# Kernel optimization log

Measured on AMD Instinct MI355X. Metric: run time of the kernel, lower is better.

The kernel has to match this reference:

```python
import jax, jax.numpy as jnp
import numpy as np

# init kwargs baked as constants: crop_height -> depth dim, crop_length -> H, crop_width -> W
CROP_D, CROP_H, CROP_W = 16, 16, 16
EXTRAP = 0.0


def setup_inputs() -> dict:
    key = jax.random.key(0)
    k1, k2, k3 = jax.random.split(key, 3)
    N, C, D, H, W = 8, 32, 64, 64, 64
    NB = 256
    image = jax.random.normal(k1, (N, C, D, H, W), dtype=jnp.float32)
    # boxes: normalized (x1, y1, z1, x2, y2, z2) with lo <= hi per axis
    raw = jax.random.uniform(k2, (NB, 3, 2), dtype=jnp.float32)
    lo = jnp.min(raw, axis=2)
    hi = jnp.max(raw, axis=2)
    boxes = jnp.concatenate([lo, hi], axis=1)  # [NB, 6]
    box_ind = jax.random.randint(k3, (NB,), 0, N, dtype=jnp.int32)
    return {"image": image, "boxes": boxes, "box_ind": box_ind}


def _coords(lo, hi, L, c):
    # lo, hi: [nb] normalized box edges; returns [nb, c] continuous source coords
    if c > 1:
        i = jnp.arange(c, dtype=lo.dtype)
        step = (hi - lo) * (L - 1) / (c - 1)          # [nb]
        return lo[:, None] * (L - 1) + i[None, :] * step[:, None]
    return (0.5 * (lo + hi) * (L - 1))[:, None]


def _lerp_idx(coord, L):
    valid = (coord >= 0) & (coord <= L - 1)
    c = jnp.clip(coord, 0, L - 1)
    i0 = jnp.floor(c).astype(jnp.int32)
    i1 = jnp.minimum(i0 + 1, L - 1)
    frac = c - i0.astype(coord.dtype)
    return i0, i1, frac, valid


def reference(image, boxes, box_ind):
    N, C, D, H, W = image.shape
    x1, y1, z1, x2, y2, z2 = [boxes[:, k] for k in range(6)]
    zc = _coords(z1, z2, D, CROP_D)  # [nb, cd]
    yc = _coords(y1, y2, H, CROP_H)  # [nb, ch]
    xc = _coords(x1, x2, W, CROP_W)  # [nb, cw]
    z0, z1i, fz, vz = _lerp_idx(zc, D)
    y0, y1i, fy, vy = _lerp_idx(yc, H)
    x0, x1i, fx, vx = _lerp_idx(xc, W)

    img = jnp.moveaxis(image, 1, -1)  # [N, D, H, W, C] -> channels-last gather
    b = box_ind[:, None, None, None]

    def g(zi, yi, xi):
        # [nb, cd, ch, cw, C]
        return img[b, zi[:, :, None, None], yi[:, None, :, None], xi[:, None, None, :], :]

    fz_ = fz[:, :, None, None, None]
    fy_ = fy[:, None, :, None, None]
    fx_ = fx[:, None, None, :, None]

    c00 = g(z0, y0, x0) * (1 - fx_) + g(z0, y0, x1i) * fx_
    c01 = g(z0, y1i, x0) * (1 - fx_) + g(z0, y1i, x1i) * fx_
    c10 = g(z1i, y0, x0) * (1 - fx_) + g(z1i, y0, x1i) * fx_
    c11 = g(z1i, y1i, x0) * (1 - fx_) + g(z1i, y1i, x1i) * fx_
    c0 = c00 * (1 - fy_) + c01 * fy_
    c1 = c10 * (1 - fy_) + c11 * fy_
    out = c0 * (1 - fz_) + c1 * fz_  # [nb, cd, ch, cw, C]

    valid = (vz[:, :, None, None] & vy[:, None, :, None] & vx[:, None, None, :])[..., None]
    out = jnp.where(valid, out, jnp.asarray(EXTRAP, out.dtype))
    return jnp.moveaxis(out, -1, 1)  # [nb, C, cd, ch, cw]
```

## Files before the change

kernel.cpp:

```cpp
#include <hip/hip_runtime.h>

#define NBOX 256
#define NC   32
#define ND   64
#define NH   64
#define NW   64
#define CD   16
#define CH   16
#define CW   16
#define NXCD 8

__global__ __launch_bounds__(256) void CropAndResize3D_89481348645400_kernel(
    const float* __restrict__ image,
    const float* __restrict__ boxes,
    const int*   __restrict__ box_ind,
    float*       __restrict__ out)
{
    const int nwg_per_xcd = (NBOX * CD) / NXCD;
    const int hw  = blockIdx.x;
    const int blk = (hw & (NXCD - 1)) * nwg_per_xcd + (hw >> 3);

    const int b = blk >> 4;
    const int z = blk & 15;
    const int t = threadIdx.x;
    const int y = t >> 4;
    const int x = t & 15;

    const float bx1 = boxes[b * 6 + 0];
    const float by1 = boxes[b * 6 + 1];
    const float bz1 = boxes[b * 6 + 2];
    const float bx2 = boxes[b * 6 + 3];
    const float by2 = boxes[b * 6 + 4];
    const float bz2 = boxes[b * 6 + 5];
    const int   n   = box_ind[b];

    const float zstep = (bz2 - bz1) * (float)(ND - 1) / (float)(CD - 1);
    const float ystep = (by2 - by1) * (float)(NH - 1) / (float)(CH - 1);
    const float xstep = (bx2 - bx1) * (float)(NW - 1) / (float)(CW - 1);
    const float zc = bz1 * (float)(ND - 1) + (float)z * zstep;
    const float yc = by1 * (float)(NH - 1) + (float)y * ystep;
    const float xc = bx1 * (float)(NW - 1) + (float)x * xstep;

    const bool valid =
        (zc >= 0.0f) && (zc <= (float)(ND - 1)) &&
        (yc >= 0.0f) && (yc <= (float)(NH - 1)) &&
        (xc >= 0.0f) && (xc <= (float)(NW - 1));

    const float zq = fminf(fmaxf(zc, 0.0f), (float)(ND - 1));
    const float yq = fminf(fmaxf(yc, 0.0f), (float)(NH - 1));
    const float xq = fminf(fmaxf(xc, 0.0f), (float)(NW - 1));
    const int z0 = (int)floorf(zq);
    const int y0 = (int)floorf(yq);
    const int x0 = (int)floorf(xq);
    const int z1 = min(z0 + 1, ND - 1);
    const int y1 = min(y0 + 1, NH - 1);
    const int x1 = min(x0 + 1, NW - 1);
    const float fz = zq - (float)z0;
    const float fy = yq - (float)y0;
    const float fx = xq - (float)x0;
    const float gz = 1.0f - fz, gy = 1.0f - fy, gx = 1.0f - fx;

    const float w000 = gz * gy * gx, w001 = gz * gy * fx;
    const float w010 = gz * fy * gx, w011 = gz * fy * fx;
    const float w100 = fz * gy * gx, w101 = fz * gy * fx;
    const float w110 = fz * fy * gx, w111 = fz * fy * fx;

    const int o00 = (z0 * NH + y0) * NW;
    const int o01 = (z0 * NH + y1) * NW;
    const int o10 = (z1 * NH + y0) * NW;
    const int o11 = (z1 * NH + y1) * NW;

    const float* img = image + (size_t)n * (NC * ND * NH * NW);
    float* op = out + (size_t)b * (NC * CD * CH * CW) + (z * CH + y) * CW + x;

    #pragma unroll 8
    for (int c = 0; c < NC; ++c) {
        const float* p = img + (size_t)c * (ND * NH * NW);
        float v = p[o00 + x0] * w000 + p[o00 + x1] * w001
                + p[o01 + x0] * w010 + p[o01 + x1] * w011
                + p[o10 + x0] * w100 + p[o10 + x1] * w101
                + p[o11 + x0] * w110 + p[o11 + x1] * w111;
        v = valid ? v : 0.0f;
        __builtin_nontemporal_store(v, op + c * (CD * CH * CW));
    }
}

extern "C" void kernel_launch(void* const* d_in, const int* in_sizes, int n_in,
                              void* d_out, int out_size, void* d_ws, size_t ws_size,
                              hipStream_t stream) {
    const float* image   = (const float*)d_in[0];
    const float* boxes   = (const float*)d_in[1];
    const int*   box_ind = (const int*)d_in[2];
    float*       out     = (float*)d_out;

    const int blocks = NBOX * CD;
    CropAndResize3D_89481348645400_kernel<<<blocks, 256, 0, stream>>>(
        image, boxes, box_ind, out);
}
```

Before: 138.1 us.

## Stage full source rows in LDS with double-buffered float4 loads per channel

Each block now cooperatively loads, per channel, the 64 needed source rows (the 16 y0/y1 row pairs at z0 and z1) as full 64-wide rows into padded shared memory using float4 loads. Threads then do their eight-tap trilinear interpolation from LDS. Loading whole rows avoids many scattered 4-byte global gathers. The next channel's loads are issued into registers while the current channel computes, which overlaps latency. The cost is fetching whole 64-wide rows even when the box spans few x columns, plus four barriers per channel pair.

```diff
diff --git a/kernel.cpp b/kernel.cpp
--- a/kernel.cpp
+++ b/kernel.cpp
@@ -9,6 +9,9 @@
 #define CH   16
 #define CW   16
 #define NXCD 8
+#define HW_  (NH * NW)
+#define DHW  (ND * NH * NW)
+#define PAD  68
 
 __global__ __launch_bounds__(256) void CropAndResize3D_89481348645400_kernel(
     const float* __restrict__ image,
@@ -16,15 +19,17 @@
     const int*   __restrict__ box_ind,
     float*       __restrict__ out)
 {
+    __shared__ float sh[64 * PAD];
+
     const int nwg_per_xcd = (NBOX * CD) / NXCD;
     const int hw  = blockIdx.x;
     const int blk = (hw & (NXCD - 1)) * nwg_per_xcd + (hw >> 3);
 
     const int b = blk >> 4;
     const int z = blk & 15;
-    const int t = threadIdx.x;
-    const int y = t >> 4;
-    const int x = t & 15;
+    const int t  = threadIdx.x;
+    const int ty = t >> 4;
+    const int tx = t & 15;
 
     const float bx1 = boxes[b * 6 + 0];
     const float by1 = boxes[b * 6 + 1];
@@ -34,55 +39,109 @@
     const float bz2 = boxes[b * 6 + 5];
     const int   n   = box_ind[b];
 
-    const float zstep = (bz2 - bz1) * (float)(ND - 1) / (float)(CD - 1);
-    const float ystep = (by2 - by1) * (float)(NH - 1) / (float)(CH - 1);
-    const float xstep = (bx2 - bx1) * (float)(NW - 1) / (float)(CW - 1);
-    const float zc = bz1 * (float)(ND - 1) + (float)z * zstep;
-    const float yc = by1 * (float)(NH - 1) + (float)y * ystep;
-    const float xc = bx1 * (float)(NW - 1) + (float)x * xstep;
+    const float zstep = (bz2 - bz1) * 63.0f / 15.0f;
+    const float ystep = (by2 - by1) * 63.0f / 15.0f;
+    const float xstep = (bx2 - bx1) * 63.0f / 15.0f;
 
-    const bool valid =
-        (zc >= 0.0f) && (zc <= (float)(ND - 1)) &&
-        (yc >= 0.0f) && (yc <= (float)(NH - 1)) &&
-        (xc >= 0.0f) && (xc <= (float)(NW - 1));
+    const float zc = bz1 * 63.0f + (float)z * zstep;
+    const bool  vz = (zc >= 0.0f) && (zc <= 63.0f);
+    const float zq = fminf(fmaxf(zc, 0.0f), 63.0f);
+    const int   z0 = (int)floorf(zq);
+    const int   z1 = min(z0 + 1, ND - 1);
+    const float fz = zq - (float)z0;
 
-    const float zq = fminf(fmaxf(zc, 0.0f), (float)(ND - 1));
-    const float yq = fminf(fmaxf(yc, 0.0f), (float)(NH - 1));
-    const float xq = fminf(fmaxf(xc, 0.0f), (float)(NW - 1));
-    const int z0 = (int)floorf(zq);
-    const int y0 = (int)floorf(yq);
-    const int x0 = (int)floorf(xq);
-    const int z1 = min(z0 + 1, ND - 1);
-    const int y1 = min(y0 + 1, NH - 1);
-    const int x1 = min(x0 + 1, NW - 1);
-    const float fz = zq - (float)z0;
-    const float fy = yq - (float)y0;
-    const float fx = xq - (float)x0;
+    const float ycf = by1 * 63.0f + (float)ty * ystep;
+    const bool  vy  = (ycf >= 0.0f) && (ycf <= 63.0f);
+    const float yq  = fminf(fmaxf(ycf, 0.0f), 63.0f);
+    const float fy  = yq - floorf(yq);
+
+    const float xcf = bx1 * 63.0f + (float)tx * xstep;
+    const bool  vx  = (xcf >= 0.0f) && (xcf <= 63.0f);
+    const float xq  = fminf(fmaxf(xcf, 0.0f), 63.0f);
+    const int   x0  = (int)floorf(xq);
+    const int   x1  = min(x0 + 1, NW - 1);
+    const float fx  = xq - (float)x0;
+
+    const bool valid = vz && vy && vx;
     const float gz = 1.0f - fz, gy = 1.0f - fy, gx = 1.0f - fx;
 
-    const float w000 = gz * gy * gx, w001 = gz * gy * fx;
-    const float w010 = gz * fy * gx, w011 = gz * fy * fx;
-    const float w100 = fz * gy * gx, w101 = fz * gy * fx;
-    const float w110 = fz * fy * gx, w111 = fz * fy * fx;
+    int soff[4];
+    int dst[4];
+    #pragma unroll
+    for (int k = 0; k < 4; ++k) {
+        const int r   = k * 16 + ty;
+        const int yo  = (r >> 1) & 15;
+        const int yc_ = r & 1;
+        const int zs  = (r >> 5) ? z1 : z0;
+        const float yco = by1 * 63.0f + (float)yo * ystep;
+        const float yqs = fminf(fmaxf(yco, 0.0f), 63.0f);
+        const int   ys0 = (int)floorf(yqs);
+        const int   ysel = yc_ ? min(ys0 + 1, NH - 1) : ys0;
+        soff[k] = zs * HW_ + ysel * NW + tx * 4;
+        dst[k]  = r * PAD + tx * 4;
+    }
 
-    const int o00 = (z0 * NH + y0) * NW;
-    const int o01 = (z0 * NH + y1) * NW;
-    const int o10 = (z1 * NH + y0) * NW;
-    const int o11 = (z1 * NH + y1) * NW;
+    const int r00 = (ty * 2 + 0) * PAD;
+    const int r01 = (ty * 2 + 1) * PAD;
+    const int r10 = (32 + ty * 2 + 0) * PAD;
+    const int r11 = (32 + ty * 2 + 1) * PAD;
 
-    const float* img = image + (size_t)n * (NC * ND * NH * NW);
-    float* op = out + (size_t)b * (NC * CD * CH * CW) + (z * CH + y) * CW + x;
+    const float* imgb = image + (size_t)n * (NC * DHW);
+    float* op = out + (size_t)b * (NC * CD * CH * CW) + (z * CH + ty) * CW + tx;
 
-    #pragma unroll 8
-    for (int c = 0; c < NC; ++c) {
-        const float* p = img + (size_t)c * (ND * NH * NW);
-        float v = p[o00 + x0] * w000 + p[o00 + x1] * w001
-                + p[o01 + x0] * w010 + p[o01 + x1] * w011
-                + p[o10 + x0] * w100 + p[o10 + x1] * w101
-                + p[o11 + x0] * w110 + p[o11 + x1] * w111;
-        v = valid ? v : 0.0f;
-        __builtin_nontemporal_store(v, op + c * (CD * CH * CW));
+    float4 A0, A1, A2, A3, B0, B1, B2, B3;
+
+    #define LOADSET(R0, R1, R2, R3, c)  do {                                   \
+        const float* pc_ = imgb + (size_t)(c) * DHW;                           \
+        R0 = *(const float4*)(pc_ + soff[0]);                                  \
+        R1 = *(const float4*)(pc_ + soff[1]);                                  \
+        R2 = *(const float4*)(pc_ + soff[2]);                                  \
+        R3 = *(const float4*)(pc_ + soff[3]);                                  \
+    } while (0)
+
+    #define WRITESET(R0, R1, R2, R3)  do {                                     \
+        *(float4*)(sh + dst[0]) = R0;                                          \
+        *(float4*)(sh + dst[1]) = R1;                                          \
+        *(float4*)(sh + dst[2]) = R2;                                          \
+        *(float4*)(sh + dst[3]) = R3;                                          \
+    } while (0)
+
+    #define COMPUTE(c)  do {                                                   \
+        const float s000 = sh[r00 + x0], s001 = sh[r00 + x1];                  \
+        const float s010 = sh[r01 + x0], s011 = sh[r01 + x1];                  \
+        const float s100 = sh[r10 + x0], s101 = sh[r10 + x1];                  \
+        const float s110 = sh[r11 + x0], s111 = sh[r11 + x1];                  \
+        const float c00 = s000 * gx + s001 * fx;                               \
+        const float c01 = s010 * gx + s011 * fx;                               \
+        const float c10 = s100 * gx + s101 * fx;                               \
+        const float c11 = s110 * gx + s111 * fx;                               \
+        const float c0  = c00 * gy + c01 * fy;                                 \
+        const float c1  = c10 * gy + c11 * fy;                                 \
+        float v = c0 * gz + c1 * fz;                                           \
+        v = valid ? v : 0.0f;                                                  \
+        __builtin_nontemporal_store(v, op + (c) * (CD * CH * CW));             \
+    } while (0)
+
+    LOADSET(A0, A1, A2, A3, 0);
+
+    #pragma unroll 2
+    for (int c = 0; c < NC; c += 2) {
+        __syncthreads();
+        WRITESET(A0, A1, A2, A3);
+        if (c + 1 < NC) LOADSET(B0, B1, B2, B3, c + 1);
+        __syncthreads();
+        COMPUTE(c);
+
+        __syncthreads();
+        WRITESET(B0, B1, B2, B3);
+        if (c + 2 < NC) LOADSET(A0, A1, A2, A3, c + 2);
+        __syncthreads();
+        COMPUTE(c + 1);
     }
+
+    #undef LOADSET
+    #undef WRITESET
+    #undef COMPUTE
 }
 
 extern "C" void kernel_launch(void* const* d_in, const int* in_sizes, int n_in,
```

New measurement: 145.8 us. 5.5% more time.
